# Optimization experiments

Hardware: AMD Instinct MI355X
Metric: run time of the kernel (lower is better)

Reference implementation:

```python
import jax, jax.numpy as jnp
import numpy as np

NUM_HEADS = 16
THETA = 10000.0


def setup_inputs() -> dict:
    key = jax.random.key(0)
    ks = jax.random.split(key, 5)
    B, S, D = 2, 2048, 1024
    scale = 1.0 / np.sqrt(D)
    return {
        "x": jax.random.normal(ks[0], (B, S, D), dtype=jnp.float32),
        "Wq": jax.random.normal(ks[1], (D, D), dtype=jnp.float32) * scale,
        "Wk": jax.random.normal(ks[2], (D, D), dtype=jnp.float32) * scale,
        "Wv": jax.random.normal(ks[3], (D, D), dtype=jnp.float32) * scale,
        "Wo": jax.random.normal(ks[4], (D, D), dtype=jnp.float32) * scale,
    }


def _rope(t, cos, sin):
    # t: [B, H, S, d_k], interleaved pair rotation.
    t1 = t[..., 0::2]
    t2 = t[..., 1::2]
    r1 = t1 * cos - t2 * sin
    r2 = t1 * sin + t2 * cos
    # re-interleave
    out = jnp.stack([r1, r2], axis=-1)
    return out.reshape(t.shape)


def reference(x, Wq, Wk, Wv, Wo):
    B, S, D = x.shape
    H = NUM_HEADS
    dk = D // H

    # projections (Linear: y = x @ W^T)
    Q = jnp.einsum("bsd,ed->bse", x, Wq).reshape(B, S, H, dk).transpose(0, 2, 1, 3)
    K = jnp.einsum("bsd,ed->bse", x, Wk).reshape(B, S, H, dk).transpose(0, 2, 1, 3)
    V = jnp.einsum("bsd,ed->bse", x, Wv).reshape(B, S, H, dk).transpose(0, 2, 1, 3)

    # RoPE angles: [S, dk/2]
    inv_freq = THETA ** (-jnp.arange(0, dk, 2, dtype=jnp.float32) / dk)
    ang = jnp.arange(S, dtype=jnp.float32)[:, None] * inv_freq[None, :]
    cos, sin = jnp.cos(ang), jnp.sin(ang)  # broadcast over [B, H, S, dk/2]
    Q = _rope(Q, cos, sin)
    K = _rope(K, cos, sin)

    # causal SDPA
    scores = jnp.einsum("bhqd,bhkd->bhqk", Q, K) / jnp.sqrt(jnp.float32(dk))
    causal = jnp.tril(jnp.ones((S, S), dtype=bool))
    scores = jnp.where(causal, scores, jnp.finfo(scores.dtype).min)
    attn = jax.nn.softmax(scores, axis=-1)
    out = jnp.einsum("bhqk,bhkd->bhqd", attn, V)

    out = out.transpose(0, 2, 1, 3).reshape(B, S, D)
    return jnp.einsum("bsd,ed->bse", out, Wo)
```

## Files before the change

kernel.cpp:

```cpp
#include <hip/hip_runtime.h>
#include <hip/hip_bf16.h>

#define B_   2
#define S_   2048
#define H_   16
#define DK_  64
#define D_   1024
#define BS_  4096
#define N3_  3072

typedef __attribute__((ext_vector_type(8))) short short8;
typedef __attribute__((ext_vector_type(4))) float floatx4;
typedef __hip_bfloat16 bf16;

__device__ inline void load_lds16(const bf16* g, bf16* l) {
    __builtin_amdgcn_global_load_lds(
        (const __attribute__((address_space(1))) void*)g,
        (__attribute__((address_space(3))) void*)l, 16, 0, 0);
}

__device__ inline unsigned int pack2bf16(float a, float b) {
    __hip_bfloat162 h = __float22bfloat162_rn(make_float2(a, b));
    return *(unsigned int*)&h;
}

__global__ void cvt_all(const float* __restrict__ x,  const float* __restrict__ wq,
                        const float* __restrict__ wk, const float* __restrict__ wv,
                        const float* __restrict__ wo,
                        bf16* __restrict__ xb, bf16* __restrict__ wcat, bf16* __restrict__ wob) {
    const int blk = blockIdx.x;
    const float* src; bf16* dst; int base;
    if (blk < 4096)      { src = x;  dst = xb;             base = blk * 1024; }
    else if (blk < 5120) { src = wq; dst = wcat;           base = (blk - 4096) * 1024; }
    else if (blk < 6144) { src = wk; dst = wcat + 1048576; base = (blk - 5120) * 1024; }
    else if (blk < 7168) { src = wv; dst = wcat + 2097152; base = (blk - 6144) * 1024; }
    else                 { src = wo; dst = wob;            base = (blk - 7168) * 1024; }
    const int i = base + threadIdx.x * 4;
    float4 v = *(const float4*)(src + i);
    *(uint2*)(dst + i) = make_uint2(pack2bf16(v.x, v.y), pack2bf16(v.z, v.w));
}

__global__ __launch_bounds__(256)
void gemm_qkv(const bf16* __restrict__ A, const bf16* __restrict__ Bw,
              bf16* __restrict__ Qr, bf16* __restrict__ Kr, bf16* __restrict__ Vt) {
    __shared__ __align__(16) bf16 lA[128 * 64];
    __shared__ __align__(16) bf16 lB[128 * 64];
    const int t = threadIdx.x;
    const int lane = t & 63, w = t >> 6;
    const int quad = lane >> 4, l16 = lane & 15;
    const int m0 = blockIdx.x * 128, n0 = blockIdx.y * 128;
    const int wm = (w & 1) * 64, wn = (w >> 1) * 64;

    floatx4 acc[4][4];
#pragma unroll
    for (int i = 0; i < 4; i++)
#pragma unroll
        for (int j = 0; j < 4; j++) acc[i][j] = (floatx4){0.f, 0.f, 0.f, 0.f};

    const int srow = t >> 3;
    const int sj   = (t & 7) ^ (srow & 7);

    for (int kt = 0; kt < D_; kt += 64) {
#pragma unroll
        for (int r = 0; r < 4; r++)
            load_lds16(A + (size_t)(m0 + r * 32 + srow) * D_ + kt + sj * 8,
                       lA + r * 2048 + t * 8);
#pragma unroll
        for (int r = 0; r < 4; r++)
            load_lds16(Bw + (size_t)(n0 + r * 32 + srow) * D_ + kt + sj * 8,
                       lB + r * 2048 + t * 8);
        __syncthreads();

#pragma unroll
        for (int kh = 0; kh < 2; kh++) {
            short8 af[4], bfr[4];
#pragma unroll
            for (int i = 0; i < 4; i++) {
                const int row = wm + i * 16 + l16;
                af[i] = *(const short8*)&lA[row * 64 + ((kh * 4 + quad) ^ (row & 7)) * 8];
            }
#pragma unroll
            for (int j = 0; j < 4; j++) {
                const int row = wn + j * 16 + l16;
                bfr[j] = *(const short8*)&lB[row * 64 + ((kh * 4 + quad) ^ (row & 7)) * 8];
            }
#pragma unroll
            for (int i = 0; i < 4; i++)
#pragma unroll
                for (int j = 0; j < 4; j++)
                    acc[i][j] = __builtin_amdgcn_mfma_f32_16x16x32_bf16(af[i], bfr[j], acc[i][j], 0, 0, 0);
        }
        __syncthreads();
    }

    if (n0 < 2 * D_) {
        const bool isQ = (n0 < D_);
        const float SC = isQ ? 0.18033688011112042f : 1.0f;
        bf16* dst = isQ ? Qr : Kr;
#pragma unroll
        for (int j = 0; j < 4; j++) {
            const int col = n0 + wn + j * 16 + l16;
            const int cc  = col & (D_ - 1);
            const int h   = cc >> 6, d = cc & 63;
            const float fr = exp2f(-(float)(d & 62) * 0.2076205059304601f)
                             * 0.15915494309189535f;
#pragma unroll
            for (int i = 0; i < 4; i++) {
                const int row0 = m0 + wm + i * 16 + quad * 4;
                const int bb = row0 >> 11, s0 = row0 & (S_ - 1);
                bf16* base = dst + (((size_t)(bb * H_ + h) * S_) + s0) * 64 + d;
#pragma unroll
                for (int r = 0; r < 4; r++) {
                    const float v = acc[i][j][r];
                    const float p = __shfl_xor(v, 1);
                    float rev = (float)(s0 + r) * fr;
                    rev -= floorf(rev);
                    const float sn = __builtin_amdgcn_sinf(rev);
                    const float cs = __builtin_amdgcn_cosf(rev);
                    const float sps = (lane & 1) ? sn : -sn;
                    base[(size_t)r * 64] = __float2bfloat16((v * cs + p * sps) * SC);
                }
            }
        }
    } else {
#pragma unroll
        for (int i = 0; i < 4; i++) {
            const int row0 = m0 + wm + i * 16 + quad * 4;
            const int bb = row0 >> 11;
            const int ss = row0 & 2047;
#pragma unroll
            for (int j = 0; j < 4; j++) {
                const int c = n0 + wn + j * 16 + l16 - 2 * D_;
                const int h = c >> 6, d = c & 63;
                *(uint2*)(Vt + (((size_t)bb * H_ + h) * 64 + d) * S_ + ss) =
                    make_uint2(pack2bf16(acc[i][j][0], acc[i][j][1]),
                               pack2bf16(acc[i][j][2], acc[i][j][3]));
            }
        }
    }
}

__global__ __launch_bounds__(512)
void attn_kernel(const bf16* __restrict__ Qr, const bf16* __restrict__ Kr,
                 const bf16* __restrict__ Vt, bf16* __restrict__ Ob) {
    __shared__ __align__(16) bf16 lK0[64 * 64], lK1[64 * 64];
    __shared__ __align__(16) bf16 lV0[64 * 64], lV1[64 * 64];
    __shared__ __align__(16) bf16 lP[8][16][36];

    const int t = threadIdx.x;
    const int w = t >> 6, lane = t & 63;
    const int quad = lane >> 4, l16 = lane & 15;

    const int lin  = (int)blockIdx.y * 16 + (int)blockIdx.x;
    const int half = lin >> 8;
    const int j    = lin & 255;
    const int bh   = j >> 3;
    const int k    = j & 7;
    const int qblk = half ? (7 - k) : (8 + k);

    const int b = bh >> 4, h = bh & 15;
    const int q0w = qblk * 128 + w * 16;
    const int q = q0w + l16;

    const bf16* Qb = Qr + (size_t)bh * S_ * 64;
    const bf16* Kb = Kr + (size_t)bh * S_ * 64;
    const bf16* Vb = Vt + (size_t)bh * 64 * S_;

    const int srow = t >> 3;
    const int sj   = (t & 7) ^ (srow & 7);
    const int swz = l16 & 7;
    const int pA = quad ^ swz;
    const int pB = (4 + quad) ^ swz;

    const bf16* qrow = Qb + (size_t)q * 64;
    short8 bq[2];
    bq[0] = *(const short8*)(qrow + quad * 8);
    bq[1] = *(const short8*)(qrow + 32 + quad * 8);

    float lacc = 0.f;
    floatx4 o[4];
#pragma unroll
    for (int ct = 0; ct < 4; ct++) o[ct] = (floatx4){0.f, 0.f, 0.f, 0.f};

    auto stage = [&](bf16* dK, bf16* dV, int kb) {
        load_lds16(Kb + (size_t)(kb + srow) * 64 + sj * 8, dK + t * 8);
        load_lds16(Vb + (size_t)srow * S_ + kb + sj * 8,   dV + t * 8);
    };

    auto computeStep = [&](const bf16* lKc, const bf16* lVc, int kb, bool need_mask) {
#pragma unroll
        for (int c = 0; c < 2; c++) {
            floatx4 s[2];
#pragma unroll
            for (int k2 = 0; k2 < 2; k2++) {
                const int kt = c * 2 + k2;
                const short8 k0 = *(const short8*)&lKc[(kt * 16 + l16) * 64 + pA * 8];
                const short8 k1 = *(const short8*)&lKc[(kt * 16 + l16) * 64 + pB * 8];
                floatx4 z = (floatx4){0.f, 0.f, 0.f, 0.f};
                z = __builtin_amdgcn_mfma_f32_16x16x32_bf16(k0, bq[0], z, 0, 0, 0);
                z = __builtin_amdgcn_mfma_f32_16x16x32_bf16(k1, bq[1], z, 0, 0, 0);
                s[k2] = z;
            }
            float rs = 0.f;
#pragma unroll
            for (int k2 = 0; k2 < 2; k2++) {
                float p[4];
#pragma unroll
                for (int r = 0; r < 4; r++) {
                    float v = s[k2][r];
                    if (need_mask) {
                        const int key = kb + (c * 2 + k2) * 16 + quad * 4 + r;
                        if (key > q) v = -1e30f;
                    }
                    p[r] = __builtin_amdgcn_exp2f(v);
                    rs += p[r];
                }
                *(uint2*)&lP[w][l16][k2 * 16 + quad * 4] =
                    make_uint2(pack2bf16(p[0], p[1]), pack2bf16(p[2], p[3]));
            }
            lacc += rs;
            const int pc = c ? pB : pA;
            const short8 bp = *(const short8*)&lP[w][l16][quad * 8];
#pragma unroll
            for (int ct = 0; ct < 4; ct++) {
                const short8 av = *(const short8*)&lVc[(ct * 16 + l16) * 64 + pc * 8];
                o[ct] = __builtin_amdgcn_mfma_f32_16x16x32_bf16(av, bp, o[ct], 0, 0, 0);
            }
        }
    };

    const int nsteps = 2 * qblk + 2;
    const int nst_w  = (q0w + 79) >> 6;
    stage(lK0, lV0, 0);
    __syncthreads();
    for (int st = 0; st < nsteps; ++st) {
        const bool even = (st & 1) == 0;
        const bf16* cK = even ? lK0 : lK1;  const bf16* cV = even ? lV0 : lV1;
        bf16* nK = even ? lK1 : lK0;        bf16* nV = even ? lV1 : lV0;
        if (st + 1 < nsteps) stage(nK, nV, (st + 1) * 64);
        if (st < nst_w) computeStep(cK, cV, st * 64, st == nst_w - 1);
        __syncthreads();
    }

    float l = lacc;
    l += __shfl_xor(l, 16);
    l += __shfl_xor(l, 32);
    const float invl = 1.0f / l;
    bf16* orow = Ob + ((size_t)(b * S_ + q) * H_ + h) * 64;
#pragma unroll
    for (int ct = 0; ct < 4; ct++)
        *(uint2*)(orow + ct * 16 + quad * 4) =
            make_uint2(pack2bf16(o[ct][0] * invl, o[ct][1] * invl),
                       pack2bf16(o[ct][2] * invl, o[ct][3] * invl));
}

__global__ __launch_bounds__(256)
void gemm_out(const bf16* __restrict__ A, const bf16* __restrict__ Bw,
              float* __restrict__ C) {
    __shared__ __align__(16) bf16 lA[128 * 64];
    __shared__ __align__(16) bf16 lB[64 * 64];
    const int t = threadIdx.x;
    const int lane = t & 63, w = t >> 6;
    const int quad = lane >> 4, l16 = lane & 15;
    const int m0 = blockIdx.x * 128, n0 = blockIdx.y * 64;
    const int wm = (w & 1) * 64, wn = (w >> 1) * 32;

    floatx4 acc[4][2];
#pragma unroll
    for (int i = 0; i < 4; i++)
#pragma unroll
        for (int j = 0; j < 2; j++) acc[i][j] = (floatx4){0.f, 0.f, 0.f, 0.f};

    const int srow = t >> 3;
    const int sj   = (t & 7) ^ (srow & 7);

    for (int kt = 0; kt < D_; kt += 64) {
#pragma unroll
        for (int r = 0; r < 4; r++)
            load_lds16(A + (size_t)(m0 + r * 32 + srow) * D_ + kt + sj * 8,
                       lA + r * 2048 + t * 8);
#pragma unroll
        for (int r = 0; r < 2; r++)
            load_lds16(Bw + (size_t)(n0 + r * 32 + srow) * D_ + kt + sj * 8,
                       lB + r * 2048 + t * 8);
        __syncthreads();

#pragma unroll
        for (int kh = 0; kh < 2; kh++) {
            short8 af[4], bfr[2];
#pragma unroll
            for (int i = 0; i < 4; i++) {
                const int row = wm + i * 16 + l16;
                af[i] = *(const short8*)&lA[row * 64 + ((kh * 4 + quad) ^ (row & 7)) * 8];
            }
#pragma unroll
            for (int j = 0; j < 2; j++) {
                const int row = wn + j * 16 + l16;
                bfr[j] = *(const short8*)&lB[row * 64 + ((kh * 4 + quad) ^ (row & 7)) * 8];
            }
#pragma unroll
            for (int i = 0; i < 4; i++)
#pragma unroll
                for (int j = 0; j < 2; j++)
                    acc[i][j] = __builtin_amdgcn_mfma_f32_16x16x32_bf16(af[i], bfr[j], acc[i][j], 0, 0, 0);
        }
        __syncthreads();
    }

#pragma unroll
    for (int i = 0; i < 4; i++) {
        const int row = m0 + wm + i * 16 + quad * 4;
#pragma unroll
        for (int j = 0; j < 2; j++) {
            const int col = n0 + wn + j * 16 + l16;
#pragma unroll
            for (int r = 0; r < 4; r++)
                C[(size_t)(row + r) * D_ + col] = acc[i][j][r];
        }
    }
}

extern "C" void kernel_launch(void* const* d_in, const int* in_sizes, int n_in,
                              void* d_out, int out_size, void* d_ws, size_t ws_size,
                              hipStream_t stream) {
    const float* x  = (const float*)d_in[0];
    const float* Wq = (const float*)d_in[1];
    const float* Wk = (const float*)d_in[2];
    const float* Wv = (const float*)d_in[3];
    const float* Wo = (const float*)d_in[4];
    float* out = (float*)d_out;

    char* ws = (char*)d_ws;
    bf16* xb   = (bf16*)(ws);
    bf16* Wcat = (bf16*)(ws + 8388608);
    bf16* Wob  = (bf16*)(ws + 14680064);
    bf16* Ob   = (bf16*)(ws + 16777216);
    bf16* Qr   = (bf16*)(ws + 41943040);
    bf16* Kr   = (bf16*)(ws + 50331648);
    bf16* Vt   = (bf16*)(ws + 58720256);

    cvt_all<<<8192, 256, 0, stream>>>(x, Wq, Wk, Wv, Wo, xb, Wcat, Wob);
    gemm_qkv<<<dim3(32, 24), 256, 0, stream>>>(xb, Wcat, Qr, Kr, Vt);
    attn_kernel<<<dim3(16, B_ * H_), 512, 0, stream>>>(Qr, Kr, Vt, Ob);
    gemm_out<<<dim3(32, 16), 256, 0, stream>>>(Ob, Wob, out);
}
```

Measured before the change: 176.7 us.

## Enlarge QKV GEMM tile to 256x192 with double-buffered LDS prefetch

The QKV projection GEMM moves from 128x128 tiles with 256 threads to 256x192 tiles with 512 threads (8 waves, each computing 64x96). It also double-buffers the LDS stages so the next k-slice's global loads are issued before the current slice's MFMAs, with one barrier per k-step. The larger tile raises arithmetic intensity and the prefetch is meant to hide load latency. In exchange the block uses about 112KB of LDS and more accumulator registers, which limits occupancy. The grid drops to 256 blocks, roughly one per CU.

```diff
diff --git a/kernel.cpp b/kernel.cpp
--- a/kernel.cpp
+++ b/kernel.cpp
@@ -40,68 +40,74 @@
     *(uint2*)(dst + i) = make_uint2(pack2bf16(v.x, v.y), pack2bf16(v.z, v.w));
 }
 
-__global__ __launch_bounds__(256)
+__global__ __launch_bounds__(512)
 void gemm_qkv(const bf16* __restrict__ A, const bf16* __restrict__ Bw,
               bf16* __restrict__ Qr, bf16* __restrict__ Kr, bf16* __restrict__ Vt) {
-    __shared__ __align__(16) bf16 lA[128 * 64];
-    __shared__ __align__(16) bf16 lB[128 * 64];
+    __shared__ __align__(16) bf16 lA[2][256 * 64];
+    __shared__ __align__(16) bf16 lB[2][192 * 64];
     const int t = threadIdx.x;
     const int lane = t & 63, w = t >> 6;
     const int quad = lane >> 4, l16 = lane & 15;
-    const int m0 = blockIdx.x * 128, n0 = blockIdx.y * 128;
-    const int wm = (w & 1) * 64, wn = (w >> 1) * 64;
-
-    floatx4 acc[4][4];
+    const int m0 = blockIdx.x * 256, n0 = blockIdx.y * 192;
+    const int wm = (w & 3) * 64, wn = (w >> 2) * 96;
+
+    floatx4 acc[4][6];
 #pragma unroll
     for (int i = 0; i < 4; i++)
 #pragma unroll
-        for (int j = 0; j < 4; j++) acc[i][j] = (floatx4){0.f, 0.f, 0.f, 0.f};
+        for (int j = 0; j < 6; j++) acc[i][j] = (floatx4){0.f, 0.f, 0.f, 0.f};
 
     const int srow = t >> 3;
     const int sj   = (t & 7) ^ (srow & 7);
 
-    for (int kt = 0; kt < D_; kt += 64) {
+    auto stage = [&](int buf, int kt) {
 #pragma unroll
         for (int r = 0; r < 4; r++)
-            load_lds16(A + (size_t)(m0 + r * 32 + srow) * D_ + kt + sj * 8,
-                       lA + r * 2048 + t * 8);
-#pragma unroll
-        for (int r = 0; r < 4; r++)
-            load_lds16(Bw + (size_t)(n0 + r * 32 + srow) * D_ + kt + sj * 8,
-                       lB + r * 2048 + t * 8);
-        __syncthreads();
-
+            load_lds16(A + (size_t)(m0 + r * 64 + srow) * D_ + kt + sj * 8,
+                       &lA[buf][r * 4096 + t * 8]);
+#pragma unroll
+        for (int r = 0; r < 3; r++)
+            load_lds16(Bw + (size_t)(n0 + r * 64 + srow) * D_ + kt + sj * 8,
+                       &lB[buf][r * 4096 + t * 8]);
+    };
+
+    stage(0, 0);
+    __syncthreads();
+    int cur = 0;
+    for (int ks = 0; ks < 16; ks++) {
+        if (ks + 1 < 16) stage(cur ^ 1, (ks + 1) * 64);
 #pragma unroll
         for (int kh = 0; kh < 2; kh++) {
-            short8 af[4], bfr[4];
+            short8 af[4], bfr[6];
 #pragma unroll
             for (int i = 0; i < 4; i++) {
                 const int row = wm + i * 16 + l16;
-                af[i] = *(const short8*)&lA[row * 64 + ((kh * 4 + quad) ^ (row & 7)) * 8];
-            }
-#pragma unroll
-            for (int j = 0; j < 4; j++) {
+                af[i] = *(const short8*)&lA[cur][row * 64 + ((kh * 4 + quad) ^ (row & 7)) * 8];
+            }
+#pragma unroll
+            for (int j = 0; j < 6; j++) {
                 const int row = wn + j * 16 + l16;
-                bfr[j] = *(const short8*)&lB[row * 64 + ((kh * 4 + quad) ^ (row & 7)) * 8];
+                bfr[j] = *(const short8*)&lB[cur][row * 64 + ((kh * 4 + quad) ^ (row & 7)) * 8];
             }
 #pragma unroll
             for (int i = 0; i < 4; i++)
 #pragma unroll
-                for (int j = 0; j < 4; j++)
+                for (int j = 0; j < 6; j++)
                     acc[i][j] = __builtin_amdgcn_mfma_f32_16x16x32_bf16(af[i], bfr[j], acc[i][j], 0, 0, 0);
         }
         __syncthreads();
-    }
-
-    if (n0 < 2 * D_) {
-        const bool isQ = (n0 < D_);
-        const float SC = isQ ? 0.18033688011112042f : 1.0f;
-        bf16* dst = isQ ? Qr : Kr;
-#pragma unroll
-        for (int j = 0; j < 4; j++) {
-            const int col = n0 + wn + j * 16 + l16;
-            const int cc  = col & (D_ - 1);
-            const int h   = cc >> 6, d = cc & 63;
+        cur ^= 1;
+    }
+
+#pragma unroll
+    for (int j = 0; j < 6; j++) {
+        const int col16 = n0 + wn + j * 16;
+        const int cls = col16 >> 10;
+        if (cls < 2) {
+            const float SC = (cls == 0) ? 0.18033688011112042f : 1.0f;
+            bf16* dst = (cls == 0) ? Qr : Kr;
+            const int cc = (col16 & (D_ - 1)) + l16;
+            const int h = cc >> 6, d = cc & 63;
             const float fr = exp2f(-(float)(d & 62) * 0.2076205059304601f)
                              * 0.15915494309189535f;
 #pragma unroll
@@ -121,17 +127,14 @@
                     base[(size_t)r * 64] = __float2bfloat16((v * cs + p * sps) * SC);
                 }
             }
-        }
-    } else {
-#pragma unroll
-        for (int i = 0; i < 4; i++) {
-            const int row0 = m0 + wm + i * 16 + quad * 4;
-            const int bb = row0 >> 11;
-            const int ss = row0 & 2047;
-#pragma unroll
-            for (int j = 0; j < 4; j++) {
-                const int c = n0 + wn + j * 16 + l16 - 2 * D_;
-                const int h = c >> 6, d = c & 63;
+        } else {
+            const int c = col16 + l16 - 2 * D_;
+            const int h = c >> 6, d = c & 63;
+#pragma unroll
+            for (int i = 0; i < 4; i++) {
+                const int row0 = m0 + wm + i * 16 + quad * 4;
+                const int bb = row0 >> 11;
+                const int ss = row0 & 2047;
                 *(uint2*)(Vt + (((size_t)bb * H_ + h) * 64 + d) * S_ + ss) =
                     make_uint2(pack2bf16(acc[i][j][0], acc[i][j][1]),
                                pack2bf16(acc[i][j][2], acc[i][j][3]));
@@ -340,7 +343,7 @@
     bf16* Vt   = (bf16*)(ws + 58720256);
 
     cvt_all<<<8192, 256, 0, stream>>>(x, Wq, Wk, Wv, Wo, xb, Wcat, Wob);
-    gemm_qkv<<<dim3(32, 24), 256, 0, stream>>>(xb, Wcat, Qr, Kr, Vt);
+    gemm_qkv<<<dim3(16, 16), 512, 0, stream>>>(xb, Wcat, Qr, Kr, Vt);
     attn_kernel<<<dim3(16, B_ * H_), 512, 0, stream>>>(Qr, Kr, Vt, Ob);
     gemm_out<<<dim3(32, 16), 256, 0, stream>>>(Ob, Wob, out);
 }
```

Result: faster. 170.0 us, median of 2 (-3.8%).
